# Kernel optimization log

Measured on AMD Instinct MI355X. Metric: run time of the kernel, lower is better.

Reference implementation:

```python
import jax, jax.numpy as jnp
import numpy as np

B, N, E = 64, 1024, 16384  # graphs, nodes per graph, edges per graph
N_ITER = 5
NORMALIZE = True
NUM_INIT_LABELS = 16


def _unique_inverse(h):
    """Equivalent of torch.unique(h, sorted=True, return_inverse=True)[1] for 1-D h."""
    order = jnp.argsort(h)
    sh = h[order]
    bnd = jnp.concatenate([jnp.zeros(1, jnp.int32), (sh[1:] != sh[:-1]).astype(jnp.int32)])
    ranks = jnp.cumsum(bnd)  # dense rank in sorted-unique order
    return jnp.zeros_like(ranks).at[order].set(ranks)


def _wl_iteration(mask, labels, hash_w):
    """One WL iteration for all graphs.
    mask: [B,N,N] bool dense adjacency (sparse-to-dense, as in the torch code)
    labels: [B,N] int32
    hash_w: [2] float32 (Linear(2,1,bias=False) weight)
    Returns new labels [B,N] int32.
    """
    w0, w1 = hash_w[0], hash_w[1]
    lab_f = labels.astype(jnp.float32)
    deg = mask.sum(-1).astype(jnp.float32)                      # [B,N] valid-neighbor count
    K = deg.max(axis=-1, keepdims=True)                         # per-graph max_neighbors
    # sum of neighbor labels (gather+reduce over the dense mask, memory-bound)
    seg = jnp.einsum('bij,bj->bi', mask.astype(jnp.float32), lab_f)  # [B,N]
    # torch builds [N,max_neighbors] rows: node label in col 0-feature, sorted
    # neighbor labels (padded with -1) in col 1-feature, hashes each pair with
    # w0*node + w1*neigh and sums over columns. Closed form (sort is sum-invariant):
    #   K*w0*node + w1*(sum_neighbors - (K - deg))
    hashed = K * w0 * lab_f + w1 * (seg + deg - K)              # [B,N]
    return jax.vmap(_unique_inverse)(hashed)


def setup_inputs() -> dict:
    key = jax.random.key(0)
    k1, k2, k3, k4 = jax.random.split(key, 4)
    edge_src = jax.random.randint(k1, (B, E), 0, N, dtype=jnp.int32)
    edge_dst = jax.random.randint(k2, (B, E), 0, N, dtype=jnp.int32)
    labels = jax.random.randint(k3, (B, N), 0, NUM_INIT_LABELS, dtype=jnp.int32)
    hash_w = jax.random.normal(k4, (2,), dtype=jnp.float32)
    return {"edge_src": edge_src, "edge_dst": edge_dst, "labels": labels, "hash_w": hash_w}


def reference(edge_src, edge_dst, labels, hash_w):
    # sparse-to-dense neighbor mask, as in the torch module
    b_idx = jnp.arange(B, dtype=jnp.int32)[:, None]
    mask = jnp.zeros((B, N, N), dtype=bool).at[b_idx, edge_src, edge_dst].set(True)

    all_labels = [labels]
    for _ in range(N_ITER):
        all_labels.append(_wl_iteration(mask, all_labels[-1], hash_w))

    # feature vectors: per graph, bincount of labels summed over all iterations.
    # Labels are always < N (unique-inverse ranks < N; initial labels < 16),
    # so N bins is a tight static upper bound for torch's max_label+1; the extra
    # zero columns do not change the Gram matrix.
    labels_all = jnp.stack(all_labels, axis=1).reshape(B, -1)   # [B, (n_iter+1)*N]
    feats = jax.vmap(lambda l: jnp.zeros((N,), jnp.float32).at[l].add(1.0))(labels_all)

    kernel = feats @ feats.T                                    # [B,B]
    if NORMALIZE:
        d = jnp.sqrt(jnp.diag(kernel))
        kernel = kernel / (d[None, :] * d[:, None])
    return kernel
```

## Files before the change

kernel.cpp:

```cpp
#include <hip/hip_runtime.h>

#define B 64
#define N 1024
#define E 16384
#define WPR 32
#define NITER 5
#define CSR_SLOTS (E + N)
#define CH_ROWS 384
#define CH_WORDS (CH_ROWS * WPR)
#define NCHUNK 3

#define FEATS_OFF 0
#define DIAG_OFF  ((size_t)B * N * 4)

__global__ void __launch_bounds__(1024) wl_mega_k(const int* __restrict__ src,
                                                  const int* __restrict__ dstp,
                                                  const int* __restrict__ lab0,
                                                  const float* __restrict__ hw,
                                                  unsigned int* __restrict__ feats,
                                                  float* __restrict__ diag) {
    __shared__ union {
        unsigned int chunk[CH_WORDS];
        struct {
            unsigned short nbr[CSR_SLOTS];
            struct {
                int hist[N];
                int scan[N];
                float grp[N];
                int flag[N];
            } pb;
        } s;
    } u;
    __shared__ int s_lab[N + 2];
    __shared__ unsigned int s_feats[N];
    __shared__ int s_wsum[16];
    __shared__ int s_kp[16];
    __shared__ float s_mn[16], s_mx[16];
    __shared__ float s_gmn, s_gmx;
    __shared__ int s_K;
    __shared__ int s_anytie;
    int b = blockIdx.x, t = threadIdx.x;
    int lane = t & 63, w = t >> 6;

    const int* sg = src + (size_t)b * E;
    const int* dg_ = dstp + (size_t)b * E;
    int es[16], ed[16];
#pragma unroll
    for (int k = 0; k < 16; ++k) {
        es[k] = sg[t + k * 1024];
        ed[k] = dg_[t + k * 1024];
    }
    int l0 = lab0[(size_t)b * N + t];
    s_lab[t] = l0;
    s_feats[t] = 0;
    if (t == 0) { s_lab[N] = 0; s_anytie = 0; }
    __syncthreads();
#pragma unroll
    for (int v = 0; v < 16; ++v) {
        unsigned long long m = __ballot(l0 == v);
        if (lane == v) {
            int c = __popcll(m);
            if (c) atomicAdd(&s_feats[v], (unsigned)c);
        }
    }

    uint4 r[8];
#pragma unroll 1
    for (int c = 0; c < NCHUNK; ++c) {
        int base = c * CH_ROWS;
#pragma unroll
        for (int k = 0; k < 3; ++k)
            ((uint4*)u.chunk)[t + k * 1024] = make_uint4(0, 0, 0, 0);
        __syncthreads();
#pragma unroll
        for (int k = 0; k < 16; ++k) {
            int rr = es[k] - base;
            if ((unsigned)rr < (unsigned)CH_ROWS) {
                int wlog = ed[k] >> 5;
                int g = wlog >> 2;
                int p = (g + rr) & 7;
                atomicOr(&u.chunk[rr * WPR + p * 4 + (wlog & 3)],
                         1u << (ed[k] & 31));
            }
        }
        __syncthreads();
        int rl = t - base;
        if ((unsigned)rl < (unsigned)CH_ROWS) {
            const uint4* row4 = (const uint4*)(u.chunk + rl * WPR);
#pragma unroll
            for (int g = 0; g < 8; ++g)
                r[g] = row4[(g + rl) & 7];
        }
        __syncthreads();
    }

    int dg = 0;
#pragma unroll
    for (int k = 0; k < 8; ++k)
        dg += __popc(r[k].x) + __popc(r[k].y) + __popc(r[k].z) + __popc(r[k].w);
    int alloc = (dg + 1) & ~1;

    int f = alloc;
#pragma unroll
    for (int d2 = 1; d2 < 64; d2 <<= 1) {
        int v = __shfl_up(f, d2);
        if (lane >= d2) f += v;
    }
    int km = dg;
#pragma unroll
    for (int o = 32; o > 0; o >>= 1) km = max(km, __shfl_down(km, o));
    if (lane == 63) s_wsum[w] = f;
    if (lane == 0)  s_kp[w] = km;
    __syncthreads();
    if (w == 0) {
        int orig = (lane < 16) ? s_wsum[lane] : 0;
        int v = orig;
#pragma unroll
        for (int d2 = 1; d2 < 16; d2 <<= 1) {
            int uu = __shfl_up(v, d2);
            if (lane >= d2) v += uu;
        }
        if (lane < 16) s_wsum[lane] = v - orig;
        int kk = (lane < 16) ? s_kp[lane] : 0;
#pragma unroll
        for (int m2 = 8; m2 >= 1; m2 >>= 1) kk = max(kk, __shfl_xor(kk, m2));
        if (lane == 0) s_K = kk;
    }
    __syncthreads();
    int start = (f - alloc) + s_wsum[w];
    u.s.pb.hist[t] = 0;
    u.s.pb.flag[t] = 0;

    {
        int idx = start;
#pragma unroll
        for (int k = 0; k < 8; ++k) {
            unsigned int wv[4] = { r[k].x, r[k].y, r[k].z, r[k].w };
#pragma unroll
            for (int c2 = 0; c2 < 4; ++c2) {
                unsigned int word = wv[c2];
                int bb = (k * 4 + c2) << 5;
                while (word) {
                    int j = __ffs(word) - 1;
                    word &= word - 1;
                    u.s.nbr[idx++] = (unsigned short)(bb + j);
                }
            }
        }
        if (dg & 1) u.s.nbr[idx] = (unsigned short)N;
    }
    float Kf = (float)s_K;
    float w0 = hw[0], w1 = hw[1];
    int pairs = alloc >> 1;
    int pstart = start >> 1;
    __syncthreads();

    for (int it = 0; it < NITER; ++it) {
        int s = 0;
        const unsigned int* nbr32 = (const unsigned int*)u.s.nbr;
        for (int k = 0; k < pairs; ++k) {
            unsigned int pr = nbr32[pstart + k];
            s += s_lab[pr & 0xFFFFu] + s_lab[pr >> 16];
        }
        float t1 = __fmul_rn(__fmul_rn(Kf, w0), (float)s_lab[t]);
        float t2 = __fmul_rn(w1, __fsub_rn(__fadd_rn((float)s, (float)dg), Kf));
        float h  = __fadd_rn(t1, t2);

        float mn = h, mx = h;
#pragma unroll
        for (int o = 32; o > 0; o >>= 1) {
            mn = fminf(mn, __shfl_down(mn, o));
            mx = fmaxf(mx, __shfl_down(mx, o));
        }
        if (lane == 0) { s_mn[w] = mn; s_mx[w] = mx; }
        __syncthreads();
        if (w == 0) {
            float a = (lane < 16) ? s_mn[lane] : 3.4e38f;
            float c = (lane < 16) ? s_mx[lane] : -3.4e38f;
#pragma unroll
            for (int m2 = 8; m2 >= 1; m2 >>= 1) {
                a = fminf(a, __shfl_xor(a, m2));
                c = fmaxf(c, __shfl_xor(c, m2));
            }
            if (lane == 0) { s_gmn = a; s_gmx = c; }
        }
        __syncthreads();
        float fmn = s_gmn;
        float span = s_gmx - fmn;
        float scale = (span > 0.f) ? (1023.0f / span) : 0.f;
        int bucket = min((int)((h - fmn) * scale), 1023);
        int off_in = atomicAdd(&u.s.pb.hist[bucket], 1);
        __syncthreads();

        f = u.s.pb.hist[t];
#pragma unroll
        for (int d2 = 1; d2 < 64; d2 <<= 1) {
            int v = __shfl_up(f, d2);
            if (lane >= d2) f += v;
        }
        if (lane == 63) s_wsum[w] = f;
        __syncthreads();
        if (w == 0) {
            int orig = (lane < 16) ? s_wsum[lane] : 0;
            int v = orig;
#pragma unroll
            for (int d2 = 1; d2 < 16; d2 <<= 1) {
                int uu = __shfl_up(v, d2);
                if (lane >= d2) v += uu;
            }
            if (lane < 16) s_wsum[lane] = v - orig;
        }
        __syncthreads();
        u.s.pb.scan[t] = f + s_wsum[w];
        __syncthreads();

        int bs = u.s.pb.scan[bucket] - u.s.pb.hist[bucket];
        int be = u.s.pb.scan[bucket];
        u.s.pb.grp[bs + off_in] = h;
        __syncthreads();

        int c = bs;
        int eq = 0;
        for (int k = bs; k < be; ++k) {
            float g = u.s.pb.grp[k];
            c += (g < h);
            eq += (g == h);
        }
        if (eq > 1) s_anytie = it + 1;
        u.s.pb.hist[t] = 0;
        __syncthreads();

        int rank;
        if (s_anytie != it + 1) {
            rank = c;
            s_lab[t] = rank;
            s_feats[rank] += 1u;
        } else {
            u.s.pb.flag[c] = 1;
            __syncthreads();
            int f2 = u.s.pb.flag[t];
#pragma unroll
            for (int d2 = 1; d2 < 64; d2 <<= 1) {
                int v = __shfl_up(f2, d2);
                if (lane >= d2) f2 += v;
            }
            if (lane == 63) s_wsum[w] = f2;
            __syncthreads();
            if (w == 0) {
                int orig = (lane < 16) ? s_wsum[lane] : 0;
                int v = orig;
#pragma unroll
                for (int d2 = 1; d2 < 16; d2 <<= 1) {
                    int uu = __shfl_up(v, d2);
                    if (lane >= d2) v += uu;
                }
                if (lane < 16) s_wsum[lane] = v - orig;
            }
            __syncthreads();
            u.s.pb.scan[t] = f2 + s_wsum[w];
            u.s.pb.flag[t] = 0;
            __syncthreads();
            rank = u.s.pb.scan[c] - 1;
            s_lab[t] = rank;
            atomicAdd(&s_feats[rank], 1u);
        }
        __syncthreads();
    }

    unsigned int fv = s_feats[t];
    feats[(size_t)b * N + t] = fv;
    int sq = (int)(fv * fv);
#pragma unroll
    for (int o = 32; o > 0; o >>= 1) sq += __shfl_down(sq, o);
    if (lane == 0) s_wsum[w] = sq;
    __syncthreads();
    if (t == 0) {
        int tot = 0;
#pragma unroll
        for (int k = 0; k < 16; ++k) tot += s_wsum[k];
        diag[b] = (float)tot;
    }
}

__global__ void __launch_bounds__(256) gram_k(const unsigned int* __restrict__ feats,
                                              const float* __restrict__ diag,
                                              float* __restrict__ out) {
    __shared__ unsigned int s_fi[N];
    int i = blockIdx.x, t = threadIdx.x;
    int lane = t & 63, w = t >> 6;
    ((uint4*)s_fi)[t] = ((const uint4*)(feats + (size_t)i * N))[t];
    __syncthreads();
    float di = diag[i];
    for (int jj = 0; jj < 16; ++jj) {
        int j = w * 16 + jj;
        const uint4* fj = (const uint4*)(feats + (size_t)j * N);
        const uint4* fi = (const uint4*)s_fi;
        int s = 0;
#pragma unroll
        for (int k = 0; k < 4; ++k) {
            uint4 vb = fj[lane + k * 64];
            uint4 va = fi[lane + k * 64];
            s += (int)(va.x * vb.x) + (int)(va.y * vb.y)
               + (int)(va.z * vb.z) + (int)(va.w * vb.w);
        }
#pragma unroll
        for (int off = 32; off > 0; off >>= 1) s += __shfl_down(s, off);
        if (lane == 0) out[i * B + j] = (float)s / sqrtf(di * diag[j]);
    }
}

extern "C" void kernel_launch(void* const* d_in, const int* in_sizes, int n_in,
                              void* d_out, int out_size, void* d_ws, size_t ws_size,
                              hipStream_t stream) {
    const int*   esrc = (const int*)d_in[0];
    const int*   edst = (const int*)d_in[1];
    const int*   lab0 = (const int*)d_in[2];
    const float* hw   = (const float*)d_in[3];

    char* ws = (char*)d_ws;
    unsigned int* feats = (unsigned int*)(ws + FEATS_OFF);
    float*        diag  = (float*)(ws + DIAG_OFF);

    wl_mega_k<<<B, 1024, 0, stream>>>(esrc, edst, lab0, hw, feats, diag);
    gram_k<<<B, 256, 0, stream>>>(feats, diag, (float*)d_out);
}
```

Baseline: 112.2 us.

## Build full adjacency bitmap at once and degree-sort nodes across threads

The adjacency bitmap is now built for all 1024 rows in one pass over a single full-size LDS buffer, replacing three chunked passes with their extra clears and barriers. Nodes are bucketed by degree and permuted so that threads in the same wavefront handle nodes with similar neighbor counts, which reduces divergence in the per-iteration neighbor-sum loop. Each thread also keeps up to 20 neighbor pairs in registers across the five WL iterations. The cost is a much larger LDS footprint, which may limit occupancy, extra register pressure, and extra setup work for the histogram and permutation.

```diff
diff --git a/kernel.cpp b/kernel.cpp
--- a/kernel.cpp
+++ b/kernel.cpp
@@ -6,9 +6,7 @@
 #define WPR 32
 #define NITER 5
 #define CSR_SLOTS (E + N)
-#define CH_ROWS 384
-#define CH_WORDS (CH_ROWS * WPR)
-#define NCHUNK 3
+#define MAXP 20
 
 #define FEATS_OFF 0
 #define DIAG_OFF  ((size_t)B * N * 4)
@@ -20,7 +18,7 @@
                                                   unsigned int* __restrict__ feats,
                                                   float* __restrict__ diag) {
     __shared__ union {
-        unsigned int chunk[CH_WORDS];
+        unsigned int chunk[N * WPR];
         struct {
             unsigned short nbr[CSR_SLOTS];
             struct {
@@ -29,6 +27,10 @@
                 float grp[N];
                 int flag[N];
             } pb;
+            int meta[N];
+            unsigned short perm[N];
+            int dh[256];
+            int dtop[256];
         } s;
     } u;
     __shared__ int s_lab[N + 2];
@@ -42,14 +44,9 @@
     int b = blockIdx.x, t = threadIdx.x;
     int lane = t & 63, w = t >> 6;
 
-    const int* sg = src + (size_t)b * E;
-    const int* dg_ = dstp + (size_t)b * E;
-    int es[16], ed[16];
-#pragma unroll
-    for (int k = 0; k < 16; ++k) {
-        es[k] = sg[t + k * 1024];
-        ed[k] = dg_[t + k * 1024];
-    }
+#pragma unroll
+    for (int k = 0; k < 8; ++k)
+        ((uint4*)u.chunk)[t + k * 1024] = make_uint4(0, 0, 0, 0);
     int l0 = lab0[(size_t)b * N + t];
     s_lab[t] = l0;
     s_feats[t] = 0;
@@ -64,35 +61,26 @@
         }
     }
 
+    const int* sg = src + (size_t)b * E;
+    const int* dg_ = dstp + (size_t)b * E;
+#pragma unroll
+    for (int k = 0; k < 16; ++k) {
+        int es = sg[t + k * 1024];
+        int ed = dg_[t + k * 1024];
+        int wlog = ed >> 5;
+        int g = wlog >> 2;
+        int p = (g + es) & 7;
+        atomicOr(&u.chunk[es * WPR + p * 4 + (wlog & 3)], 1u << (ed & 31));
+    }
+    __syncthreads();
     uint4 r[8];
-#pragma unroll 1
-    for (int c = 0; c < NCHUNK; ++c) {
-        int base = c * CH_ROWS;
-#pragma unroll
-        for (int k = 0; k < 3; ++k)
-            ((uint4*)u.chunk)[t + k * 1024] = make_uint4(0, 0, 0, 0);
-        __syncthreads();
-#pragma unroll
-        for (int k = 0; k < 16; ++k) {
-            int rr = es[k] - base;
-            if ((unsigned)rr < (unsigned)CH_ROWS) {
-                int wlog = ed[k] >> 5;
-                int g = wlog >> 2;
-                int p = (g + rr) & 7;
-                atomicOr(&u.chunk[rr * WPR + p * 4 + (wlog & 3)],
-                         1u << (ed[k] & 31));
-            }
-        }
-        __syncthreads();
-        int rl = t - base;
-        if ((unsigned)rl < (unsigned)CH_ROWS) {
-            const uint4* row4 = (const uint4*)(u.chunk + rl * WPR);
-#pragma unroll
-            for (int g = 0; g < 8; ++g)
-                r[g] = row4[(g + rl) & 7];
-        }
-        __syncthreads();
-    }
+    {
+        const uint4* row4 = (const uint4*)(u.chunk + t * WPR);
+#pragma unroll
+        for (int g = 0; g < 8; ++g)
+            r[g] = row4[(g + t) & 7];
+    }
+    __syncthreads();
 
     int dg = 0;
 #pragma unroll
@@ -130,6 +118,7 @@
     int start = (f - alloc) + s_wsum[w];
     u.s.pb.hist[t] = 0;
     u.s.pb.flag[t] = 0;
+    if (t < 256) u.s.dh[t] = 0;
 
     {
         int idx = start;
@@ -149,21 +138,63 @@
         }
         if (dg & 1) u.s.nbr[idx] = (unsigned short)N;
     }
+    u.s.meta[t] = (start << 11) | dg;
     float Kf = (float)s_K;
     float w0 = hw[0], w1 = hw[1];
-    int pairs = alloc >> 1;
-    int pstart = start >> 1;
-    __syncthreads();
+    __syncthreads();
+
+    atomicAdd(&u.s.dh[min(dg, 255)], 1);
+    __syncthreads();
+    if (w == 0) {
+        int h0 = u.s.dh[lane * 4], h1 = u.s.dh[lane * 4 + 1];
+        int h2 = u.s.dh[lane * 4 + 2], h3 = u.s.dh[lane * 4 + 3];
+        int c1 = h0 + h1, c2 = c1 + h2, c3 = c2 + h3;
+        int ex = c3;
+#pragma unroll
+        for (int d2 = 1; d2 < 64; d2 <<= 1) {
+            int v = __shfl_up(ex, d2);
+            if (lane >= d2) ex += v;
+        }
+        ex -= c3;
+        u.s.dtop[lane * 4]     = N - (ex + h0);
+        u.s.dtop[lane * 4 + 1] = N - (ex + c1);
+        u.s.dtop[lane * 4 + 2] = N - (ex + c2);
+        u.s.dtop[lane * 4 + 3] = N - (ex + c3);
+    }
+    __syncthreads();
+    {
+        int pos = atomicAdd(&u.s.dtop[min(dg, 255)], 1);
+        u.s.perm[pos] = (unsigned short)t;
+    }
+    __syncthreads();
+    int v_node = u.s.perm[t];
+    int mv = u.s.meta[v_node];
+    int vdeg = mv & 2047;
+    int vpstart = (mv >> 11) >> 1;
+    int vpairs = ((vdeg + 1) & ~1) >> 1;
+    int lab_reg = s_lab[v_node];
+    const unsigned int* nbr32 = (const unsigned int*)u.s.nbr;
+    unsigned int pw[MAXP];
+#pragma unroll
+    for (int k = 0; k < MAXP; ++k) {
+        unsigned int pk = 0u;
+        if (k < vpairs) pk = nbr32[vpstart + k];
+        pw[k] = pk;
+    }
 
     for (int it = 0; it < NITER; ++it) {
-        int s = 0;
-        const unsigned int* nbr32 = (const unsigned int*)u.s.nbr;
-        for (int k = 0; k < pairs; ++k) {
-            unsigned int pr = nbr32[pstart + k];
-            s += s_lab[pr & 0xFFFFu] + s_lab[pr >> 16];
-        }
-        float t1 = __fmul_rn(__fmul_rn(Kf, w0), (float)s_lab[t]);
-        float t2 = __fmul_rn(w1, __fsub_rn(__fadd_rn((float)s, (float)dg), Kf));
+        int ssum = 0;
+#pragma unroll
+        for (int k = 0; k < MAXP; ++k) if (k < vpairs) {
+            unsigned int pr = pw[k];
+            ssum += s_lab[pr & 0xFFFFu] + s_lab[pr >> 16];
+        }
+        for (int k = MAXP; k < vpairs; ++k) {
+            unsigned int pr = nbr32[vpstart + k];
+            ssum += s_lab[pr & 0xFFFFu] + s_lab[pr >> 16];
+        }
+        float t1 = __fmul_rn(__fmul_rn(Kf, w0), (float)lab_reg);
+        float t2 = __fmul_rn(w1, __fsub_rn(__fadd_rn((float)ssum, (float)vdeg), Kf));
         float h  = __fadd_rn(t1, t2);
 
         float mn = h, mx = h;
@@ -233,7 +264,8 @@
         int rank;
         if (s_anytie != it + 1) {
             rank = c;
-            s_lab[t] = rank;
+            s_lab[v_node] = rank;
+            lab_reg = rank;
             s_feats[rank] += 1u;
         } else {
             u.s.pb.flag[c] = 1;
@@ -261,7 +293,8 @@
             u.s.pb.flag[t] = 0;
             __syncthreads();
             rank = u.s.pb.scan[c] - 1;
-            s_lab[t] = rank;
+            s_lab[v_node] = rank;
+            lab_reg = rank;
             atomicAdd(&s_feats[rank], 1u);
         }
         __syncthreads();
```

New measurement: 110.5 us. About the same (-1.5%).
